# Optimization experiments

Hardware: AMD Instinct MI355X
Metric: run time of the kernel (lower is better)

The kernel has to match this reference:

```python
import jax, jax.numpy as jnp
import numpy as np


def conv3x3(x, w, b):
    # x: [B,1,H,W], w: [1,1,3,3] (OIHW), b: [1]; stride 1, padding 1
    y = jax.lax.conv_general_dilated(x, w, (1, 1), 'SAME',
                                     dimension_numbers=('NCHW', 'OIHW', 'NCHW'))
    return y + b[0]


def avg_pool(x, k):
    B, C, H, W = x.shape
    return x.reshape(B, C, H // k, k, W // k, k).mean(axis=(3, 5))


def nearest_up(x, k):
    # nearest-neighbor upsample by integer factor k (matches torch 'nearest')
    return jnp.repeat(jnp.repeat(x, k, axis=2), k, axis=3)


def conv1x1(x, w):
    # x: [B,3,H,W], w: [1,3,1,1] -> [B,1,H,W]
    return jnp.einsum('bchw,oc->bohw', x, w[:, :, 0, 0])


def setup_inputs() -> dict:
    key = jax.random.key(0)
    ks = jax.random.split(key, 16)
    B, H, W = 8, 512, 512
    std = 0.005
    inp = {
        'x':          jax.random.normal(ks[0], (B, 1, H, W), jnp.float32),
        'downSample': jax.random.normal(ks[1], (B, 1, H // 2, W // 2), jnp.float32),
        'upSample':   jax.random.normal(ks[2], (B, 1, 2 * H, 2 * W), jnp.float32),
        'BU':         jax.random.normal(ks[3], (B, 1, H, W), jnp.float32),
        'BUdown':     jax.random.normal(ks[4], (B, 1, H // 2, W // 2), jnp.float32),
        'BUup':       jax.random.normal(ks[5], (B, 1, 2 * H, 2 * W), jnp.float32),
        'convAx': std * jax.random.normal(ks[6], (1, 1, 3, 3), jnp.float32),
        'biasx':  std * jax.random.normal(ks[7], (1,), jnp.float32),
        'convAd': std * jax.random.normal(ks[8], (1, 1, 3, 3), jnp.float32),
        'biasd':  std * jax.random.normal(ks[9], (1,), jnp.float32),
        'convAu': std * jax.random.normal(ks[10], (1, 1, 3, 3), jnp.float32),
        'biasu':  std * jax.random.normal(ks[11], (1,), jnp.float32),
        'conv1x1_x': std * jax.random.normal(ks[12], (1, 3, 1, 1), jnp.float32),
        'conv1x1_d': std * jax.random.normal(ks[13], (1, 3, 1, 1), jnp.float32),
        'conv1x1_u': std * jax.random.normal(ks[14], (1, 3, 1, 1), jnp.float32),
    }
    return inp


def reference(x, downSample, upSample, BU, BUdown, BUup,
              convAx, biasx, convAd, biasd, convAu, biasu,
              conv1x1_x, conv1x1_d, conv1x1_u):
    # 5 iterations of conv3x3 + residual add + clamp(-1,1) per pyramid level
    for _ in range(5):
        x = jnp.clip(conv3x3(x, convAx, biasx) + BU, -1.0, 1.0)
        downSample = jnp.clip(conv3x3(downSample, convAd, biasd) + BUdown, -1.0, 1.0)
        upSample = jnp.clip(conv3x3(upSample, convAu, biasu) + BUup, -1.0, 1.0)
    # cross-scale fusion: resample all three levels to each level and concat
    newx = jnp.concatenate([avg_pool(upSample, 2), x, nearest_up(downSample, 2)], axis=1)
    newUp = jnp.concatenate([upSample, nearest_up(x, 2), nearest_up(downSample, 4)], axis=1)
    newDown = jnp.concatenate([avg_pool(upSample, 4), avg_pool(x, 2), downSample], axis=1)
    x_out = conv1x1(newx, conv1x1_x)
    down_out = conv1x1(newDown, conv1x1_d)
    up_out = conv1x1(newUp, conv1x1_u)
    return (x_out, down_out, up_out)
```

## Files before the change

### kernel.cpp

```cpp
#include <hip/hip_runtime.h>

#define NBATCH 8
#define TW 64
#define TH 32
#define SROWS 42
#define SQUADS 20
#define STRDQ 80
#define NSTRIP 180
#define NTHR 192

__device__ __forceinline__ void acc_row(float4& v, float L, float4 m, float R,
                                        float ka, float kb, float kc) {
    v.x += ka * L   + kb * m.x + kc * m.y;
    v.y += ka * m.x + kb * m.y + kc * m.z;
    v.z += ka * m.y + kb * m.z + kc * m.w;
    v.w += ka * m.z + kb * m.w + kc * R;
}

__global__ __launch_bounds__(NTHR, 4) void conv5_all(
    const float* __restrict__ srcU, const float* __restrict__ buU,
    const float* __restrict__ wtU, const float* __restrict__ bsU,
    const float* __restrict__ srcX, const float* __restrict__ buX,
    const float* __restrict__ wtX, const float* __restrict__ bsX,
    const float* __restrict__ srcD, const float* __restrict__ buD,
    const float* __restrict__ wtD, const float* __restrict__ bsD,
    float* __restrict__ dstU, float* __restrict__ dstX, float* __restrict__ dstD)
{
    __shared__ __align__(16) float bufA[SROWS * STRDQ];
    __shared__ __align__(16) float bufB[SROWS * STRDQ];

    const int tid = threadIdx.x;
    const int blk = blockIdx.x;

    const float* src; const float* BU; const float* wt; const float* bs;
    float* dst; int HW; int tx, ty, b;
    if (blk < 4096) {
        src = srcU; BU = buU; wt = wtU; bs = bsU; dst = dstU; HW = 1024;
        b = blk >> 9; int rem = blk & 511; ty = rem >> 4; tx = rem & 15;
    } else if (blk < 5120) {
        int t = blk - 4096;
        src = srcX; BU = buX; wt = wtX; bs = bsX; dst = dstX; HW = 512;
        b = t >> 7; int rem = t & 127; ty = rem >> 3; tx = rem & 7;
    } else {
        int t = blk - 5120;
        src = srcD; BU = buD; wt = wtD; bs = bsD; dst = dstD; HW = 256;
        b = t >> 5; int rem = t & 31; ty = rem >> 2; tx = rem & 3;
    }
    const int bh0 = ty * TH, bw0 = tx * TW;
    const long base = (long)b * HW * HW;

    for (int q = tid; q < SROWS * SQUADS; q += NTHR) {
        int r = q / SQUADS, cq = q - r * SQUADS;
        int gh = bh0 + r - 5;
        int gw = bw0 + (cq << 2) - 8;
        float4 v = {0.0f, 0.0f, 0.0f, 0.0f};
        if ((unsigned)gh < (unsigned)HW) {
            const float* gp = src + base + (long)gh * HW + gw;
            if (gw >= 0 && gw + 3 < HW) {
                v = *(const float4*)gp;
            } else {
                if ((unsigned)(gw + 0) < (unsigned)HW) v.x = gp[0];
                if ((unsigned)(gw + 1) < (unsigned)HW) v.y = gp[1];
                if ((unsigned)(gw + 2) < (unsigned)HW) v.z = gp[2];
                if ((unsigned)(gw + 3) < (unsigned)HW) v.w = gp[3];
            }
        }
        *(float4*)&bufA[r * STRDQ + (cq << 2)] = v;
    }

    const float k00 = wt[0], k01 = wt[1], k02 = wt[2];
    const float k10 = wt[3], k11 = wt[4], k12 = wt[5];
    const float k20 = wt[6], k21 = wt[7], k22 = wt[8];
    const float bias = bs[0];

    const bool act = (tid < NSTRIP);
    int sc = act ? tid : 0;
    int rp = sc / 9, j = sc - rp * 9;
    const int qbase = (2 * rp) * STRDQ + 8 * j;

    float4 wf0, wf1;
    {
        float* p0 = (float*)&wf0; float* p1 = (float*)&wf1;
        #pragma unroll
        for (int k = 0; k < 4; ++k) {
            p0[k] = ((unsigned)(bw0 + 8 * j - 4 + k) < (unsigned)HW) ? 1.0f : 0.0f;
            p1[k] = ((unsigned)(bw0 + 8 * j + k)     < (unsigned)HW) ? 1.0f : 0.0f;
        }
    }
    float hf[2];
    float4 bu0[2], bu1[2];
    #pragma unroll
    for (int i = 0; i < 2; ++i) {
        int gh = bh0 + 2 * rp - 4 + i;
        bool hok = act && ((unsigned)gh < (unsigned)HW);
        hf[i] = hok ? 1.0f : 0.0f;
        float* b0 = (float*)&bu0[i]; float* b1 = (float*)&bu1[i];
        #pragma unroll
        for (int k = 0; k < 4; ++k) {
            int gw0 = bw0 + 8 * j - 4 + k;
            int gw1 = bw0 + 8 * j + k;
            b0[k] = (hok && (unsigned)gw0 < (unsigned)HW)
                        ? (BU[base + (long)gh * HW + gw0] + bias) : 0.0f;
            b1[k] = (hok && (unsigned)gw1 < (unsigned)HW)
                        ? (BU[base + (long)gh * HW + gw1] + bias) : 0.0f;
        }
    }

    float* cur = bufA;
    float* nxt = bufB;

    for (int it = 0; it < 5; ++it) {
        __syncthreads();
        if (act) {
            float4 q[4][4];
            const float* bp = cur + qbase;
            #pragma unroll
            for (int r = 0; r < 4; ++r) {
                q[r][0] = *(const float4*)(bp + r * STRDQ);
                q[r][1] = *(const float4*)(bp + r * STRDQ + 4);
                q[r][2] = *(const float4*)(bp + r * STRDQ + 8);
                q[r][3] = *(const float4*)(bp + r * STRDQ + 12);
            }
            float* wp = nxt + qbase;
            #pragma unroll
            for (int i = 0; i < 2; ++i) {
                float4 v0 = bu0[i];
                float4 v1 = bu1[i];
                acc_row(v0, q[i][0].w,     q[i][1],     q[i][2].x,     k00, k01, k02);
                acc_row(v0, q[i + 1][0].w, q[i + 1][1], q[i + 1][2].x, k10, k11, k12);
                acc_row(v0, q[i + 2][0].w, q[i + 2][1], q[i + 2][2].x, k20, k21, k22);
                acc_row(v1, q[i][1].w,     q[i][2],     q[i][3].x,     k00, k01, k02);
                acc_row(v1, q[i + 1][1].w, q[i + 1][2], q[i + 1][3].x, k10, k11, k12);
                acc_row(v1, q[i + 2][1].w, q[i + 2][2], q[i + 2][3].x, k20, k21, k22);
                float m = hf[i];
                v0.x = fminf(1.0f, fmaxf(-1.0f, v0.x)) * (m * wf0.x);
                v0.y = fminf(1.0f, fmaxf(-1.0f, v0.y)) * (m * wf0.y);
                v0.z = fminf(1.0f, fmaxf(-1.0f, v0.z)) * (m * wf0.z);
                v0.w = fminf(1.0f, fmaxf(-1.0f, v0.w)) * (m * wf0.w);
                v1.x = fminf(1.0f, fmaxf(-1.0f, v1.x)) * (m * wf1.x);
                v1.y = fminf(1.0f, fmaxf(-1.0f, v1.y)) * (m * wf1.y);
                v1.z = fminf(1.0f, fmaxf(-1.0f, v1.z)) * (m * wf1.z);
                v1.w = fminf(1.0f, fmaxf(-1.0f, v1.w)) * (m * wf1.w);
                *(float4*)(wp + (i + 1) * STRDQ + 4) = v0;
                *(float4*)(wp + (i + 1) * STRDQ + 8) = v1;
            }
        }
        float* t = cur; cur = nxt; nxt = t;
    }
    __syncthreads();

    for (int i2 = tid; i2 < TH * (TW / 4); i2 += NTHR) {
        int r = i2 >> 4;
        int cq = i2 & 15;
        float4 v = *(const float4*)&cur[(r + 5) * STRDQ + 8 + (cq << 2)];
        *(float4*)&dst[base + (long)(bh0 + r) * HW + bw0 + (cq << 2)] = v;
    }
}

__global__ __launch_bounds__(256) void fuse_all(
    const float* __restrict__ X,
    const float* __restrict__ D,
    const float* __restrict__ U,
    const float* __restrict__ cx,
    const float* __restrict__ cd,
    const float* __restrict__ cu,
    float* __restrict__ xo, float* __restrict__ dno, float* __restrict__ upo)
{
    const int total = NBATCH << 16;
    int idx = blockIdx.x * blockDim.x + threadIdx.x;
    if (idx >= total) return;
    int wd = idx & 255;
    int hd = (idx >> 8) & 255;
    int b  = idx >> 16;

    const float cx0 = cx[0], cx1 = cx[1], cx2 = cx[2];
    const float cd0 = cd[0], cd1 = cd[1], cd2 = cd[2];
    const float cu0 = cu[0], cu1 = cu[1], cu2 = cu[2];

    int ub = (b << 20) + ((hd << 2) << 10) + (wd << 2);
    float4 u0 = *(const float4*)&U[ub];
    float4 u1 = *(const float4*)&U[ub + 1024];
    float4 u2 = *(const float4*)&U[ub + 2048];
    float4 u3 = *(const float4*)&U[ub + 3072];
    int xb = (b << 18) + ((hd << 1) << 9) + (wd << 1);
    float2 x0 = *(const float2*)&X[xb];
    float2 x1 = *(const float2*)&X[xb + 512];
    float dv = D[idx];

    float p00 = 0.25f * (u0.x + u0.y + u1.x + u1.y);
    float p01 = 0.25f * (u0.z + u0.w + u1.z + u1.w);
    float p10 = 0.25f * (u2.x + u2.y + u3.x + u3.y);
    float p11 = 0.25f * (u2.z + u2.w + u3.z + u3.w);
    float pu4 = 0.25f * (p00 + p01 + p10 + p11);
    float px2 = 0.25f * (x0.x + x0.y + x1.x + x1.y);

    dno[idx] = cd0 * pu4 + cd1 * px2 + cd2 * dv;

    float2 xo0, xo1;
    xo0.x = cx0 * p00 + cx1 * x0.x + cx2 * dv;
    xo0.y = cx0 * p01 + cx1 * x0.y + cx2 * dv;
    xo1.x = cx0 * p10 + cx1 * x1.x + cx2 * dv;
    xo1.y = cx0 * p11 + cx1 * x1.y + cx2 * dv;
    *(float2*)&xo[xb]       = xo0;
    *(float2*)&xo[xb + 512] = xo1;

    float4 o0, o1, o2, o3;
    o0.x = cu0 * u0.x + cu1 * x0.x + cu2 * dv;
    o0.y = cu0 * u0.y + cu1 * x0.x + cu2 * dv;
    o0.z = cu0 * u0.z + cu1 * x0.y + cu2 * dv;
    o0.w = cu0 * u0.w + cu1 * x0.y + cu2 * dv;
    o1.x = cu0 * u1.x + cu1 * x0.x + cu2 * dv;
    o1.y = cu0 * u1.y + cu1 * x0.x + cu2 * dv;
    o1.z = cu0 * u1.z + cu1 * x0.y + cu2 * dv;
    o1.w = cu0 * u1.w + cu1 * x0.y + cu2 * dv;
    o2.x = cu0 * u2.x + cu1 * x1.x + cu2 * dv;
    o2.y = cu0 * u2.y + cu1 * x1.x + cu2 * dv;
    o2.z = cu0 * u2.z + cu1 * x1.y + cu2 * dv;
    o2.w = cu0 * u2.w + cu1 * x1.y + cu2 * dv;
    o3.x = cu0 * u3.x + cu1 * x1.x + cu2 * dv;
    o3.y = cu0 * u3.y + cu1 * x1.x + cu2 * dv;
    o3.z = cu0 * u3.z + cu1 * x1.y + cu2 * dv;
    o3.w = cu0 * u3.w + cu1 * x1.y + cu2 * dv;
    *(float4*)&upo[ub]        = o0;
    *(float4*)&upo[ub + 1024] = o1;
    *(float4*)&upo[ub + 2048] = o2;
    *(float4*)&upo[ub + 3072] = o3;
}

extern "C" void kernel_launch(void* const* d_in, const int* in_sizes, int n_in,
                              void* d_out, int out_size, void* d_ws, size_t ws_size,
                              hipStream_t stream)
{
    const float* x    = (const float*)d_in[0];
    const float* down = (const float*)d_in[1];
    const float* up   = (const float*)d_in[2];
    const float* BUx  = (const float*)d_in[3];
    const float* BUd  = (const float*)d_in[4];
    const float* BUu  = (const float*)d_in[5];
    const float* wAx  = (const float*)d_in[6];
    const float* bx   = (const float*)d_in[7];
    const float* wAd  = (const float*)d_in[8];
    const float* bd   = (const float*)d_in[9];
    const float* wAu  = (const float*)d_in[10];
    const float* bu   = (const float*)d_in[11];
    const float* c1x  = (const float*)d_in[12];
    const float* c1d  = (const float*)d_in[13];
    const float* c1u  = (const float*)d_in[14];

    float* out = (float*)d_out;
    float* ws  = (float*)d_ws;

    const int NX = NBATCH * 512 * 512;
    const int ND = NBATCH * 256 * 256;

    float* wsX = ws;
    float* wsD = ws + NX;
    float* wsU = ws + NX + ND;
    float* outX = out;
    float* outD = out + NX;
    float* outU = out + NX + ND;

    conv5_all<<<5376, NTHR, 0, stream>>>(
        up,   BUu, wAu, bu,
        x,    BUx, wAx, bx,
        down, BUd, wAd, bd,
        wsU, wsX, wsD);

    fuse_all<<<(ND + 255) / 256, 256, 0, stream>>>(wsX, wsD, wsU, c1x, c1d, c1u,
                                                   outX, outD, outU);
}
```

Measured before the change: 235.4 us.

## Swizzle shared-memory tile layout to avoid LDS bank conflicts, vectorize BU loads

Widens the LDS row stride to 96 floats and rotates each row pair's float4 slots by a row-dependent offset, with per-thread read and write offsets precomputed into registers. The aim is to cut bank conflicts on the strided float4 reads and writes in the five-iteration stencil loop. The residual BU preload now uses two float4 loads when the span is in bounds instead of scalar loads. In exchange, LDS use per block grows, which may lower occupancy, and 24 offset registers are added per thread.

```diff
diff --git a/kernel.cpp b/kernel.cpp
--- a/kernel.cpp
+++ b/kernel.cpp
@@ -5,9 +5,15 @@
 #define TH 32
 #define SROWS 42
 #define SQUADS 20
-#define STRDQ 80
+#define STRDQ 96
 #define NSTRIP 180
 #define NTHR 192
+
+__device__ __forceinline__ int lofs(int R, int q) {
+    int p = q + (3 * (R >> 1)) % 24;
+    if (p >= 24) p -= 24;
+    return R * STRDQ + (p << 2);
+}
 
 __device__ __forceinline__ void acc_row(float4& v, float L, float4 m, float R,
                                         float ka, float kb, float kc) {
@@ -49,8 +55,8 @@
     const int bh0 = ty * TH, bw0 = tx * TW;
     const long base = (long)b * HW * HW;
 
-    for (int q = tid; q < SROWS * SQUADS; q += NTHR) {
-        int r = q / SQUADS, cq = q - r * SQUADS;
+    for (int s = tid; s < SROWS * SQUADS; s += NTHR) {
+        int r = s / SQUADS, cq = s - r * SQUADS;
         int gh = bh0 + r - 5;
         int gw = bw0 + (cq << 2) - 8;
         float4 v = {0.0f, 0.0f, 0.0f, 0.0f};
@@ -65,7 +71,7 @@
                 if ((unsigned)(gw + 3) < (unsigned)HW) v.w = gp[3];
             }
         }
-        *(float4*)&bufA[r * STRDQ + (cq << 2)] = v;
+        *(float4*)&bufA[lofs(r, cq)] = v;
     }
 
     const float k00 = wt[0], k01 = wt[1], k02 = wt[2];
@@ -76,7 +82,19 @@
     const bool act = (tid < NSTRIP);
     int sc = act ? tid : 0;
     int rp = sc / 9, j = sc - rp * 9;
-    const int qbase = (2 * rp) * STRDQ + 8 * j;
+
+    int rdo[4][4];
+    #pragma unroll
+    for (int r = 0; r < 4; ++r)
+        #pragma unroll
+        for (int c = 0; c < 4; ++c)
+            rdo[r][c] = lofs(2 * rp + r, 2 * j + c);
+    int wro[2][2];
+    #pragma unroll
+    for (int i = 0; i < 2; ++i) {
+        wro[i][0] = lofs(2 * rp + 1 + i, 2 * j + 1);
+        wro[i][1] = lofs(2 * rp + 1 + i, 2 * j + 2);
+    }
 
     float4 wf0, wf1;
     {
@@ -94,15 +112,22 @@
         int gh = bh0 + 2 * rp - 4 + i;
         bool hok = act && ((unsigned)gh < (unsigned)HW);
         hf[i] = hok ? 1.0f : 0.0f;
-        float* b0 = (float*)&bu0[i]; float* b1 = (float*)&bu1[i];
-        #pragma unroll
-        for (int k = 0; k < 4; ++k) {
-            int gw0 = bw0 + 8 * j - 4 + k;
-            int gw1 = bw0 + 8 * j + k;
-            b0[k] = (hok && (unsigned)gw0 < (unsigned)HW)
-                        ? (BU[base + (long)gh * HW + gw0] + bias) : 0.0f;
-            b1[k] = (hok && (unsigned)gw1 < (unsigned)HW)
-                        ? (BU[base + (long)gh * HW + gw1] + bias) : 0.0f;
+        int gw0 = bw0 + 8 * j - 4;
+        const float* bp = BU + base + (long)gh * HW + gw0;
+        if (hok && gw0 >= 0 && gw0 + 7 < HW) {
+            float4 a = *(const float4*)bp;
+            float4 c = *(const float4*)(bp + 4);
+            bu0[i] = {a.x + bias, a.y + bias, a.z + bias, a.w + bias};
+            bu1[i] = {c.x + bias, c.y + bias, c.z + bias, c.w + bias};
+        } else {
+            float* b0 = (float*)&bu0[i]; float* b1 = (float*)&bu1[i];
+            #pragma unroll
+            for (int k = 0; k < 4; ++k) {
+                int w0 = gw0 + k;
+                int w1 = gw0 + 4 + k;
+                b0[k] = (hok && (unsigned)w0 < (unsigned)HW) ? (bp[k] + bias)     : 0.0f;
+                b1[k] = (hok && (unsigned)w1 < (unsigned)HW) ? (bp[k + 4] + bias) : 0.0f;
+            }
         }
     }
 
@@ -113,15 +138,11 @@
         __syncthreads();
         if (act) {
             float4 q[4][4];
-            const float* bp = cur + qbase;
             #pragma unroll
-            for (int r = 0; r < 4; ++r) {
-                q[r][0] = *(const float4*)(bp + r * STRDQ);
-                q[r][1] = *(const float4*)(bp + r * STRDQ + 4);
-                q[r][2] = *(const float4*)(bp + r * STRDQ + 8);
-                q[r][3] = *(const float4*)(bp + r * STRDQ + 12);
-            }
-            float* wp = nxt + qbase;
+            for (int r = 0; r < 4; ++r)
+                #pragma unroll
+                for (int c = 0; c < 4; ++c)
+                    q[r][c] = *(const float4*)(cur + rdo[r][c]);
             #pragma unroll
             for (int i = 0; i < 2; ++i) {
                 float4 v0 = bu0[i];
@@ -141,8 +162,8 @@
                 v1.y = fminf(1.0f, fmaxf(-1.0f, v1.y)) * (m * wf1.y);
                 v1.z = fminf(1.0f, fmaxf(-1.0f, v1.z)) * (m * wf1.z);
                 v1.w = fminf(1.0f, fmaxf(-1.0f, v1.w)) * (m * wf1.w);
-                *(float4*)(wp + (i + 1) * STRDQ + 4) = v0;
-                *(float4*)(wp + (i + 1) * STRDQ + 8) = v1;
+                *(float4*)(nxt + wro[i][0]) = v0;
+                *(float4*)(nxt + wro[i][1]) = v1;
             }
         }
         float* t = cur; cur = nxt; nxt = t;
@@ -152,7 +173,7 @@
     for (int i2 = tid; i2 < TH * (TW / 4); i2 += NTHR) {
         int r = i2 >> 4;
         int cq = i2 & 15;
-        float4 v = *(const float4*)&cur[(r + 5) * STRDQ + 8 + (cq << 2)];
+        float4 v = *(const float4*)&cur[lofs(r + 5, cq + 2)];
         *(float4*)&dst[base + (long)(bh0 + r) * HW + bw0 + (cq << 2)] = v;
     }
 }
```

Result: faster. 217.8 us (-7.5%).
